# Kernel tuning notes

Hardware: AMD Instinct MI355X
Metric: run time of the kernel (lower is better)

## Reference

```python
import jax, jax.numpy as jnp
import numpy as np

B, N, D, H = 2, 4096, 256, 8
HD = D // H
NEG_SLOPE = 0.01
LN_EPS = 1e-5


def setup_inputs() -> dict:
    key = jax.random.key(0)
    ks = jax.random.split(key, 6)
    s = 1.0 / np.sqrt(D)
    return {
        "h": jax.random.normal(ks[0], (B, N, D), dtype=jnp.float32),
        "W_l": jax.random.normal(ks[1], (D, D), dtype=jnp.float32) * s,
        "W_r": jax.random.normal(ks[2], (D, D), dtype=jnp.float32) * s,
        "a_l": jax.random.normal(ks[3], (HD,), dtype=jnp.float32) * s,
        "a_r": jax.random.normal(ks[4], (HD,), dtype=jnp.float32) * s,
        "W_final": jax.random.normal(ks[5], (D, D), dtype=jnp.float32) * s,
        "ln_g": jnp.ones((D,), dtype=jnp.float32),
        "ln_b": jnp.zeros((D,), dtype=jnp.float32),
    }


def _leaky(x):
    return jnp.where(x >= 0, x, NEG_SLOPE * x)


def reference(h, W_l, W_r, a_l, a_r, W_final, ln_g, ln_b):
    b, n, d = h.shape
    # projections -> [b, H, n, HD]
    fl = (h @ W_l).reshape(b, n, H, HD).transpose(0, 2, 1, 3)
    fr = (h @ W_r).reshape(b, n, H, HD).transpose(0, 2, 1, 3)
    # additive GAT-style scores: [b, H, n] each, broadcast to [b, H, n, n]
    sl = jnp.einsum("bhnd,d->bhn", _leaky(fl), a_l)
    sr = jnp.einsum("bhnd,d->bhn", _leaky(fr), a_r)
    score = sl[..., :, None] + sr[..., None, :]  # [b, H, n, n]
    attn = jnp.mean(score, axis=1)  # pre-softmax mean over heads: [b, n, n]
    p = jax.nn.softmax(score, axis=-1)  # dropout is identity (eval / p=0)
    context = jnp.einsum("bhij,bhjd->bhid", p, fr)  # [b, H, n, HD]
    h_sa = context.transpose(0, 2, 1, 3).reshape(b, n, d)
    fh = h_sa @ W_final
    x = h + fh
    mu = jnp.mean(x, axis=-1, keepdims=True)
    var = jnp.mean(jnp.square(x - mu), axis=-1, keepdims=True)
    h_out = (x - mu) * jax.lax.rsqrt(var + LN_EPS) * ln_g + ln_b
    return (h_out, attn)
```

## Files before the change

kernel.cpp:

```cpp
#include <hip/hip_runtime.h>
#include <hip/hip_bf16.h>

#define BATCH 2
#define SEQ   4096
#define DIM   256
#define HEADS 8
#define HDIM  32
#define M_ROWS (BATCH * SEQ)
#define JCHUNK 32
#define NCHUNK (SEQ / JCHUNK)
#define CTXBLKS (BATCH * NCHUNK)
#define FPSCALE 4294967296.0

typedef short bf16x8 __attribute__((ext_vector_type(8)));
typedef unsigned short u16x8 __attribute__((ext_vector_type(8)));
typedef float f32x4 __attribute__((ext_vector_type(4)));

static __device__ inline unsigned short f2bf(float x) {
  union { float f; unsigned u; } v; v.f = x;
  unsigned r = v.u + 0x7FFF + ((v.u >> 16) & 1);
  return (unsigned short)(r >> 16);
}

__global__ __launch_bounds__(256) void k_prep(const float* __restrict__ Wl,
                                              const float* __restrict__ Wr,
                                              unsigned short* __restrict__ Wt,
                                              unsigned long long* __restrict__ yacc,
                                              unsigned long long* __restrict__ wacc) {
  if (blockIdx.y == 0) {
    const int idx = blockIdx.x * 256 + threadIdx.x;
    yacc[2 * idx] = 0ull;
    yacc[2 * idx + 1] = 0ull;
    if (idx < BATCH * HEADS) wacc[idx] = 0ull;
  }
  __shared__ float tile[32][33];
  const int k0 = blockIdx.x * 32;
  const int n0 = blockIdx.y * 32;
  const int t = threadIdx.x;
  const float* W = (n0 < 256) ? Wl : Wr;
  const int nb = n0 & 255;
  {
    const int r = t >> 3;
    const int c = (t & 7) * 4;
    const float4 v = *(const float4*)(&W[(size_t)(k0 + r) * DIM + nb + c]);
    tile[r][c + 0] = v.x; tile[r][c + 1] = v.y;
    tile[r][c + 2] = v.z; tile[r][c + 3] = v.w;
  }
  __syncthreads();
  {
    const int nl = t >> 3;
    const int kl = (t & 7) * 4;
    ushort4 o;
    o.x = f2bf(tile[kl + 0][nl]); o.y = f2bf(tile[kl + 1][nl]);
    o.z = f2bf(tile[kl + 2][nl]); o.w = f2bf(tile[kl + 3][nl]);
    *(ushort4*)(&Wt[(size_t)(n0 + nl) * DIM + k0 + kl]) = o;
  }
}

__global__ __launch_bounds__(512) void k_gemm_fused(
    const float* __restrict__ A, const unsigned short* __restrict__ Wt,
    const float* __restrict__ a_l, const float* __restrict__ a_r,
    float* __restrict__ fr, float* __restrict__ sr,
    float* __restrict__ msl, float* __restrict__ msr) {
  __shared__ unsigned short As[64 * 32];
  __shared__ unsigned short Bs[256 * 32];
  __shared__ float red[64][8];

  const int bid = blockIdx.x;
  const int isR = bid & 1;
  const int bm  = bid >> 1;
  const int m0 = bm * 64;
  const int n0 = isR * 256;

  const int t = threadIdx.x;
  const int lane = t & 63;
  const int wid = t >> 6;

  f32x4 acc[4][2];
  #pragma unroll
  for (int i = 0; i < 4; ++i)
    #pragma unroll
    for (int j = 0; j < 2; ++j) acc[i][j] = (f32x4){0.f, 0.f, 0.f, 0.f};

  for (int k0 = 0; k0 < DIM; k0 += 32) {
    if (t < 256) {
      const int row = t >> 2;
      const int kc = t & 3;
      const int slot = kc ^ ((row >> 1) & 3);
      const float4 a0 = *(const float4*)(&A[(size_t)(m0 + row) * DIM + k0 + kc * 8]);
      const float4 a1 = *(const float4*)(&A[(size_t)(m0 + row) * DIM + k0 + kc * 8 + 4]);
      u16x8 pa;
      pa[0] = f2bf(a0.x); pa[1] = f2bf(a0.y); pa[2] = f2bf(a0.z); pa[3] = f2bf(a0.w);
      pa[4] = f2bf(a1.x); pa[5] = f2bf(a1.y); pa[6] = f2bf(a1.z); pa[7] = f2bf(a1.w);
      *(u16x8*)((char*)As + row * 64 + slot * 16) = pa;
    }
    #pragma unroll
    for (int p = 0; p < 2; ++p) {
      const int task = t + p * 512;
      const int row = task >> 2;
      const int kc = task & 3;
      const int slot = kc ^ ((row >> 1) & 3);
      const u16x8 pb = *(const u16x8*)(&Wt[(size_t)(n0 + row) * DIM + k0 + kc * 8]);
      *(u16x8*)((char*)Bs + row * 64 + slot * 16) = pb;
    }
    __syncthreads();

    bf16x8 af[4], bfr[2];
    #pragma unroll
    for (int mr = 0; mr < 4; ++mr) {
      const int ra = mr * 16 + (lane & 15);
      const int sl = (lane >> 4) ^ ((ra >> 1) & 3);
      af[mr] = *(const bf16x8*)((const char*)As + ra * 64 + sl * 16);
    }
    #pragma unroll
    for (int nr = 0; nr < 2; ++nr) {
      const int cb = wid * 32 + nr * 16 + (lane & 15);
      const int sl = (lane >> 4) ^ ((cb >> 1) & 3);
      bfr[nr] = *(const bf16x8*)((const char*)Bs + cb * 64 + sl * 16);
    }
    #pragma unroll
    for (int mr = 0; mr < 4; ++mr)
      #pragma unroll
      for (int nr = 0; nr < 2; ++nr)
        acc[mr][nr] = __builtin_amdgcn_mfma_f32_16x16x32_bf16(af[mr], bfr[nr], acc[mr][nr], 0, 0, 0);
    __syncthreads();
  }

  const float* av = isR ? a_r : a_l;
  const int b = m0 >> 12;
  const int nbase = m0 & 4095;

  #pragma unroll
  for (int mr = 0; mr < 4; ++mr) {
    #pragma unroll
    for (int r = 0; r < 4; ++r) {
      float p = 0.f;
      #pragma unroll
      for (int nr = 0; nr < 2; ++nr) {
        float x = acc[mr][nr][r];
        x = x >= 0.f ? x : 0.01f * x;
        p = fmaf(x, av[nr * 16 + (lane & 15)], p);
      }
      #pragma unroll
      for (int o = 1; o < 16; o <<= 1) p += __shfl_xor(p, o, 16);
      if ((lane & 15) == 0) {
        const int rl = mr * 16 + (lane >> 4) * 4 + r;
        red[rl][wid] = p;
        if (isR) sr[((size_t)(b * HEADS + wid)) * SEQ + nbase + rl] = p;
      }
    }
  }
  __syncthreads();
  if (t < 64) {
    float s = 0.f;
    #pragma unroll
    for (int h2 = 0; h2 < 8; ++h2) s += red[t][h2];
    (isR ? msr : msl)[m0 + t] = s * 0.125f;
  }
  if (isR) {
    #pragma unroll
    for (int mr = 0; mr < 4; ++mr)
      #pragma unroll
      for (int nr = 0; nr < 2; ++nr) {
        const int col = wid * 32 + nr * 16 + (lane & 15);
        #pragma unroll
        for (int r = 0; r < 4; ++r) {
          const int row = m0 + mr * 16 + (lane >> 4) * 4 + r;
          fr[(size_t)row * DIM + col] = acc[mr][nr][r];
        }
      }
  }
}

__global__ __launch_bounds__(256) void k_mega(const float* __restrict__ sr,
                                              const float* __restrict__ fr,
                                              const float* __restrict__ Wf,
                                              const float* __restrict__ msl,
                                              const float* __restrict__ msr,
                                              unsigned long long* __restrict__ yacc,
                                              unsigned long long* __restrict__ wacc,
                                              float* __restrict__ attn) {
  const int blk = blockIdx.x;
  const int t = threadIdx.x;

  if (blk < CTXBLKS) {
    __shared__ float ws_[HEADS][JCHUNK];
    __shared__ float cps[DIM];
    const int b  = blk >> 7;
    const int jc = blk & 127;
    const int j0 = jc * JCHUNK;
    {
      const int h2 = t >> 5, jj = t & 31;
      float e = expf(sr[((size_t)(b * HEADS + h2)) * SEQ + j0 + jj]);
      ws_[h2][jj] = e;
      float s = e;
      #pragma unroll
      for (int o = 16; o > 0; o >>= 1) s += __shfl_xor(s, o, 32);
      if (jj == 0)
        atomicAdd(&wacc[b * HEADS + h2],
                  (unsigned long long)__double2ll_rn((double)s * FPSCALE));
    }
    __syncthreads();
    {
      const int h2 = t >> 5;
      const float* frb = fr + (size_t)(b * SEQ + j0) * DIM + t;
      float accv = 0.f;
      #pragma unroll 8
      for (int jj = 0; jj < JCHUNK; ++jj)
        accv = fmaf(ws_[h2][jj], frb[(size_t)jj * DIM], accv);
      cps[t] = accv;
    }
    __syncthreads();
    #pragma unroll
    for (int h2 = 0; h2 < HEADS; ++h2) {
      float yh = 0.f;
      #pragma unroll 8
      for (int d = 0; d < HDIM; ++d)
        yh = fmaf(cps[h2 * HDIM + d], Wf[(size_t)(h2 * HDIM + d) * DIM + t], yh);
      atomicAdd(&yacc[(size_t)(b * HEADS + h2) * DIM + t],
                (unsigned long long)__double2ll_rn((double)yh * FPSCALE));
    }
  } else {
    const int pr = blk - CTXBLKS;
    const int row0 = pr * 2;
    const int b = row0 >> 12;
    const float v0 = msl[row0];
    const float v1 = msl[row0 + 1];
    const f32x4* mr4 = (const f32x4*)(msr + ((size_t)b << 12));
    f32x4* dst0 = (f32x4*)(attn + ((size_t)row0 << 12));
    f32x4* dst1 = (f32x4*)(attn + ((size_t)(row0 + 1) << 12));
    #pragma unroll
    for (int q = 0; q < 4; ++q) {
      const f32x4 m4 = mr4[q * 256 + t];
      __builtin_nontemporal_store(m4 + v0, &dst0[q * 256 + t]);
      __builtin_nontemporal_store(m4 + v1, &dst1[q * 256 + t]);
    }
  }
}

__global__ __launch_bounds__(256) void k_ln(const float* __restrict__ h,
                                            const unsigned long long* __restrict__ yacc,
                                            const unsigned long long* __restrict__ wacc,
                                            const float* __restrict__ g,
                                            const float* __restrict__ bb,
                                            float* __restrict__ out) {
  const int pr = blockIdx.x;
  const int row0 = pr * 2;
  const int b = row0 >> 12;
  const int t = threadIdx.x;

  float fh = 0.f;
  #pragma unroll
  for (int h2 = 0; h2 < HEADS; ++h2) {
    const double yv = (double)(long long)yacc[(size_t)(b * HEADS + h2) * DIM + t];
    const double wv = (double)(long long)wacc[b * HEADS + h2];
    fh += (float)(yv / wv);
  }

  const float x0 = h[(size_t)row0 * DIM + t] + fh;
  const float x1 = h[(size_t)(row0 + 1) * DIM + t] + fh;
  float s10 = x0, s20 = x0 * x0, s11 = x1, s21 = x1 * x1;
  #pragma unroll
  for (int o = 32; o > 0; o >>= 1) {
    s10 += __shfl_xor(s10, o, 64);
    s20 += __shfl_xor(s20, o, 64);
    s11 += __shfl_xor(s11, o, 64);
    s21 += __shfl_xor(s21, o, 64);
  }
  __shared__ float r1[2][4], r2[2][4];
  if ((t & 63) == 0) {
    r1[0][t >> 6] = s10; r2[0][t >> 6] = s20;
    r1[1][t >> 6] = s11; r2[1][t >> 6] = s21;
  }
  __syncthreads();
  const float gs = g[t], bs = bb[t];
  {
    const float s1 = r1[0][0] + r1[0][1] + r1[0][2] + r1[0][3];
    const float s2 = r2[0][0] + r2[0][1] + r2[0][2] + r2[0][3];
    const float mu = s1 * (1.f / 256.f);
    const float var = s2 * (1.f / 256.f) - mu * mu;
    const float rs = rsqrtf(var + 1e-5f);
    out[(size_t)row0 * DIM + t] = (x0 - mu) * rs * gs + bs;
  }
  {
    const float s1 = r1[1][0] + r1[1][1] + r1[1][2] + r1[1][3];
    const float s2 = r2[1][0] + r2[1][1] + r2[1][2] + r2[1][3];
    const float mu = s1 * (1.f / 256.f);
    const float var = s2 * (1.f / 256.f) - mu * mu;
    const float rs = rsqrtf(var + 1e-5f);
    out[(size_t)(row0 + 1) * DIM + t] = (x1 - mu) * rs * gs + bs;
  }
}

extern "C" void kernel_launch(void* const* d_in, const int* in_sizes, int n_in,
                              void* d_out, int out_size, void* d_ws, size_t ws_size,
                              hipStream_t stream) {
  const float* h  = (const float*)d_in[0];
  const float* Wl = (const float*)d_in[1];
  const float* Wr = (const float*)d_in[2];
  const float* al = (const float*)d_in[3];
  const float* ar = (const float*)d_in[4];
  const float* Wf = (const float*)d_in[5];
  const float* g  = (const float*)d_in[6];
  const float* bb = (const float*)d_in[7];
  float* out = (float*)d_out;

  unsigned long long* yacc = (unsigned long long*)d_ws;
  unsigned long long* wacc = yacc + BATCH * HEADS * DIM;
  float* fr  = (float*)(wacc + BATCH * HEADS);
  float* srs = fr + (size_t)M_ROWS * DIM;
  float* msl = srs + BATCH * HEADS * SEQ;
  float* msr = msl + M_ROWS;
  unsigned short* Wt = (unsigned short*)(msr + M_ROWS);

  k_prep<<<dim3(8, 16), 256, 0, stream>>>(Wl, Wr, Wt, yacc, wacc);
  k_gemm_fused<<<256, 512, 0, stream>>>(h, Wt, al, ar, fr, srs, msl, msr);
  k_mega<<<CTXBLKS + M_ROWS / 2, 256, 0, stream>>>(srs, fr, Wf, msl, msr,
                                                   yacc, wacc,
                                                   out + (size_t)M_ROWS * DIM);
  k_ln<<<M_ROWS / 2, 256, 0, stream>>>(h, yacc, wacc, g, bb, out);
}
```

Baseline: 68.53 us.

## Double-buffer GEMM smem, move attn write into LN kernel, enlarge context chunk

Adds register-prefetched double buffering of the A/B tiles in the projection GEMM, so global loads for the next k-step overlap MFMA work and one barrier per step is removed. The context reduction moves to its own kernel with 64-row chunks, which halves the block count and the atomic traffic. The large attn broadcast write moves into the LayerNorm kernel, which now runs one row per block. This trades a parallel mega-kernel for fewer atomics and a combined output pass, but the attn write no longer overlaps the context computation.

Result: faster. 61.87 us (-9.7%).

```diff
diff --git a/kernel.cpp b/kernel.cpp
--- a/kernel.cpp
+++ b/kernel.cpp
@@ -7,7 +7,7 @@
 #define HEADS 8
 #define HDIM  32
 #define M_ROWS (BATCH * SEQ)
-#define JCHUNK 32
+#define JCHUNK 64
 #define NCHUNK (SEQ / JCHUNK)
 #define CTXBLKS (BATCH * NCHUNK)
 #define FPSCALE 4294967296.0
@@ -62,8 +62,8 @@
     const float* __restrict__ a_l, const float* __restrict__ a_r,
     float* __restrict__ fr, float* __restrict__ sr,
     float* __restrict__ msl, float* __restrict__ msr) {
-  __shared__ unsigned short As[64 * 32];
-  __shared__ unsigned short Bs[256 * 32];
+  __shared__ unsigned short As2[2][64 * 32];
+  __shared__ unsigned short Bs2[2][256 * 32];
   __shared__ float red[64][8];
 
   const int bid = blockIdx.x;
@@ -76,53 +76,79 @@
   const int lane = t & 63;
   const int wid = t >> 6;
 
+  const int arow = t >> 2;
+  const int akc  = t & 3;
+  const int aslot = akc ^ ((arow >> 1) & 3);
+  const int brow = t >> 2;
+  const int bkc  = t & 3;
+  const int bslot = bkc ^ ((brow >> 1) & 3);
+
+  float4 a0r, a1r;
+  u16x8 b0r, b1r;
+
+  if (t < 256) {
+    a0r = *(const float4*)(&A[(size_t)(m0 + arow) * DIM + akc * 8]);
+    a1r = *(const float4*)(&A[(size_t)(m0 + arow) * DIM + akc * 8 + 4]);
+  }
+  b0r = *(const u16x8*)(&Wt[(size_t)(n0 + brow) * DIM + bkc * 8]);
+  b1r = *(const u16x8*)(&Wt[(size_t)(n0 + 128 + brow) * DIM + bkc * 8]);
+  if (t < 256) {
+    u16x8 pa;
+    pa[0] = f2bf(a0r.x); pa[1] = f2bf(a0r.y); pa[2] = f2bf(a0r.z); pa[3] = f2bf(a0r.w);
+    pa[4] = f2bf(a1r.x); pa[5] = f2bf(a1r.y); pa[6] = f2bf(a1r.z); pa[7] = f2bf(a1r.w);
+    *(u16x8*)((char*)As2[0] + arow * 64 + aslot * 16) = pa;
+  }
+  *(u16x8*)((char*)Bs2[0] + brow * 64 + bslot * 16) = b0r;
+  *(u16x8*)((char*)Bs2[0] + (128 + brow) * 64 + bslot * 16) = b1r;
+  __syncthreads();
+
   f32x4 acc[4][2];
   #pragma unroll
   for (int i = 0; i < 4; ++i)
     #pragma unroll
     for (int j = 0; j < 2; ++j) acc[i][j] = (f32x4){0.f, 0.f, 0.f, 0.f};
 
-  for (int k0 = 0; k0 < DIM; k0 += 32) {
-    if (t < 256) {
-      const int row = t >> 2;
-      const int kc = t & 3;
-      const int slot = kc ^ ((row >> 1) & 3);
-      const float4 a0 = *(const float4*)(&A[(size_t)(m0 + row) * DIM + k0 + kc * 8]);
-      const float4 a1 = *(const float4*)(&A[(size_t)(m0 + row) * DIM + k0 + kc * 8 + 4]);
-      u16x8 pa;
-      pa[0] = f2bf(a0.x); pa[1] = f2bf(a0.y); pa[2] = f2bf(a0.z); pa[3] = f2bf(a0.w);
-      pa[4] = f2bf(a1.x); pa[5] = f2bf(a1.y); pa[6] = f2bf(a1.z); pa[7] = f2bf(a1.w);
-      *(u16x8*)((char*)As + row * 64 + slot * 16) = pa;
-    }
-    #pragma unroll
-    for (int p = 0; p < 2; ++p) {
-      const int task = t + p * 512;
-      const int row = task >> 2;
-      const int kc = task & 3;
-      const int slot = kc ^ ((row >> 1) & 3);
-      const u16x8 pb = *(const u16x8*)(&Wt[(size_t)(n0 + row) * DIM + k0 + kc * 8]);
-      *(u16x8*)((char*)Bs + row * 64 + slot * 16) = pb;
-    }
-    __syncthreads();
+  for (int ks = 0; ks < 8; ++ks) {
+    const int cur = ks & 1;
+    if (ks < 7) {
+      const int k0 = (ks + 1) * 32;
+      if (t < 256) {
+        a0r = *(const float4*)(&A[(size_t)(m0 + arow) * DIM + k0 + akc * 8]);
+        a1r = *(const float4*)(&A[(size_t)(m0 + arow) * DIM + k0 + akc * 8 + 4]);
+      }
+      b0r = *(const u16x8*)(&Wt[(size_t)(n0 + brow) * DIM + k0 + bkc * 8]);
+      b1r = *(const u16x8*)(&Wt[(size_t)(n0 + 128 + brow) * DIM + k0 + bkc * 8]);
+    }
 
     bf16x8 af[4], bfr[2];
     #pragma unroll
     for (int mr = 0; mr < 4; ++mr) {
       const int ra = mr * 16 + (lane & 15);
       const int sl = (lane >> 4) ^ ((ra >> 1) & 3);
-      af[mr] = *(const bf16x8*)((const char*)As + ra * 64 + sl * 16);
+      af[mr] = *(const bf16x8*)((const char*)As2[cur] + ra * 64 + sl * 16);
     }
     #pragma unroll
     for (int nr = 0; nr < 2; ++nr) {
       const int cb = wid * 32 + nr * 16 + (lane & 15);
       const int sl = (lane >> 4) ^ ((cb >> 1) & 3);
-      bfr[nr] = *(const bf16x8*)((const char*)Bs + cb * 64 + sl * 16);
+      bfr[nr] = *(const bf16x8*)((const char*)Bs2[cur] + cb * 64 + sl * 16);
     }
     #pragma unroll
     for (int mr = 0; mr < 4; ++mr)
       #pragma unroll
       for (int nr = 0; nr < 2; ++nr)
         acc[mr][nr] = __builtin_amdgcn_mfma_f32_16x16x32_bf16(af[mr], bfr[nr], acc[mr][nr], 0, 0, 0);
+
+    if (ks < 7) {
+      if (t < 256) {
+        u16x8 pa;
+        pa[0] = f2bf(a0r.x); pa[1] = f2bf(a0r.y); pa[2] = f2bf(a0r.z); pa[3] = f2bf(a0r.w);
+        pa[4] = f2bf(a1r.x); pa[5] = f2bf(a1r.y); pa[6] = f2bf(a1r.z); pa[7] = f2bf(a1r.w);
+        *(u16x8*)((char*)As2[cur ^ 1] + arow * 64 + aslot * 16) = pa;
+      }
+      *(u16x8*)((char*)Bs2[cur ^ 1] + brow * 64 + bslot * 16) = b0r;
+      *(u16x8*)((char*)Bs2[cur ^ 1] + (128 + brow) * 64 + bslot * 16) = b1r;
+    }
     __syncthreads();
   }
 
@@ -172,123 +198,102 @@
   }
 }
 
-__global__ __launch_bounds__(256) void k_mega(const float* __restrict__ sr,
-                                              const float* __restrict__ fr,
-                                              const float* __restrict__ Wf,
-                                              const float* __restrict__ msl,
-                                              const float* __restrict__ msr,
-                                              unsigned long long* __restrict__ yacc,
-                                              unsigned long long* __restrict__ wacc,
-                                              float* __restrict__ attn) {
+__global__ __launch_bounds__(256) void k_ctx(const float* __restrict__ sr,
+                                             const float* __restrict__ fr,
+                                             const float* __restrict__ Wf,
+                                             unsigned long long* __restrict__ yacc,
+                                             unsigned long long* __restrict__ wacc) {
   const int blk = blockIdx.x;
+  const int b  = blk >> 6;
+  const int jc = blk & 63;
+  const int j0 = jc * JCHUNK;
   const int t = threadIdx.x;
-
-  if (blk < CTXBLKS) {
-    __shared__ float ws_[HEADS][JCHUNK];
-    __shared__ float cps[DIM];
-    const int b  = blk >> 7;
-    const int jc = blk & 127;
-    const int j0 = jc * JCHUNK;
-    {
-      const int h2 = t >> 5, jj = t & 31;
-      float e = expf(sr[((size_t)(b * HEADS + h2)) * SEQ + j0 + jj]);
-      ws_[h2][jj] = e;
-      float s = e;
-      #pragma unroll
-      for (int o = 16; o > 0; o >>= 1) s += __shfl_xor(s, o, 32);
-      if (jj == 0)
-        atomicAdd(&wacc[b * HEADS + h2],
-                  (unsigned long long)__double2ll_rn((double)s * FPSCALE));
-    }
-    __syncthreads();
-    {
-      const int h2 = t >> 5;
-      const float* frb = fr + (size_t)(b * SEQ + j0) * DIM + t;
-      float accv = 0.f;
-      #pragma unroll 8
-      for (int jj = 0; jj < JCHUNK; ++jj)
-        accv = fmaf(ws_[h2][jj], frb[(size_t)jj * DIM], accv);
-      cps[t] = accv;
-    }
-    __syncthreads();
-    #pragma unroll
-    for (int h2 = 0; h2 < HEADS; ++h2) {
-      float yh = 0.f;
-      #pragma unroll 8
-      for (int d = 0; d < HDIM; ++d)
-        yh = fmaf(cps[h2 * HDIM + d], Wf[(size_t)(h2 * HDIM + d) * DIM + t], yh);
-      atomicAdd(&yacc[(size_t)(b * HEADS + h2) * DIM + t],
-                (unsigned long long)__double2ll_rn((double)yh * FPSCALE));
-    }
-  } else {
-    const int pr = blk - CTXBLKS;
-    const int row0 = pr * 2;
-    const int b = row0 >> 12;
-    const float v0 = msl[row0];
-    const float v1 = msl[row0 + 1];
-    const f32x4* mr4 = (const f32x4*)(msr + ((size_t)b << 12));
-    f32x4* dst0 = (f32x4*)(attn + ((size_t)row0 << 12));
-    f32x4* dst1 = (f32x4*)(attn + ((size_t)(row0 + 1) << 12));
-    #pragma unroll
-    for (int q = 0; q < 4; ++q) {
-      const f32x4 m4 = mr4[q * 256 + t];
-      __builtin_nontemporal_store(m4 + v0, &dst0[q * 256 + t]);
-      __builtin_nontemporal_store(m4 + v1, &dst1[q * 256 + t]);
-    }
-  }
-}
-
-__global__ __launch_bounds__(256) void k_ln(const float* __restrict__ h,
-                                            const unsigned long long* __restrict__ yacc,
-                                            const unsigned long long* __restrict__ wacc,
-                                            const float* __restrict__ g,
-                                            const float* __restrict__ bb,
-                                            float* __restrict__ out) {
-  const int pr = blockIdx.x;
-  const int row0 = pr * 2;
-  const int b = row0 >> 12;
+  __shared__ float ws_[HEADS][JCHUNK];
+  __shared__ float cps[DIM];
+
+  {
+    const int h2 = t >> 5, jj = t & 31;
+    const float* sb = sr + ((size_t)(b * HEADS + h2)) * SEQ + j0;
+    const float e0 = expf(sb[jj]);
+    const float e1 = expf(sb[jj + 32]);
+    ws_[h2][jj] = e0;
+    ws_[h2][jj + 32] = e1;
+    float s = e0 + e1;
+    #pragma unroll
+    for (int o = 16; o > 0; o >>= 1) s += __shfl_xor(s, o, 32);
+    if (jj == 0)
+      atomicAdd(&wacc[b * HEADS + h2],
+                (unsigned long long)__double2ll_rn((double)s * FPSCALE));
+  }
+  __syncthreads();
+  {
+    const int h2 = t >> 5;
+    const float* frb = fr + (size_t)(b * SEQ + j0) * DIM + t;
+    float accv = 0.f;
+    #pragma unroll 8
+    for (int jj = 0; jj < JCHUNK; ++jj)
+      accv = fmaf(ws_[h2][jj], frb[(size_t)jj * DIM], accv);
+    cps[t] = accv;
+  }
+  __syncthreads();
+  #pragma unroll
+  for (int h3 = 0; h3 < HEADS; ++h3) {
+    float yh = 0.f;
+    #pragma unroll 8
+    for (int d = 0; d < HDIM; ++d)
+      yh = fmaf(cps[h3 * HDIM + d], Wf[(size_t)(h3 * HDIM + d) * DIM + t], yh);
+    atomicAdd(&yacc[(size_t)(b * HEADS + h3) * DIM + t],
+              (unsigned long long)__double2ll_rn((double)yh * FPSCALE));
+  }
+}
+
+__global__ __launch_bounds__(256) void k_ln_attn(const float* __restrict__ h,
+                                                 const unsigned long long* __restrict__ yacc,
+                                                 const unsigned long long* __restrict__ wacc,
+                                                 const float* __restrict__ g,
+                                                 const float* __restrict__ bb,
+                                                 const float* __restrict__ msl,
+                                                 const float* __restrict__ msr,
+                                                 float* __restrict__ out,
+                                                 float* __restrict__ attn) {
+  const int row = blockIdx.x;
+  const int b = row >> 12;
   const int t = threadIdx.x;
+  __shared__ float winv[HEADS];
+  if (t < HEADS)
+    winv[t] = (float)(1.0 / (double)(long long)wacc[b * HEADS + t]);
+  __syncthreads();
 
   float fh = 0.f;
   #pragma unroll
-  for (int h2 = 0; h2 < HEADS; ++h2) {
-    const double yv = (double)(long long)yacc[(size_t)(b * HEADS + h2) * DIM + t];
-    const double wv = (double)(long long)wacc[b * HEADS + h2];
-    fh += (float)(yv / wv);
-  }
-
-  const float x0 = h[(size_t)row0 * DIM + t] + fh;
-  const float x1 = h[(size_t)(row0 + 1) * DIM + t] + fh;
-  float s10 = x0, s20 = x0 * x0, s11 = x1, s21 = x1 * x1;
+  for (int h2 = 0; h2 < HEADS; ++h2)
+    fh = fmaf((float)(long long)yacc[(size_t)(b * HEADS + h2) * DIM + t],
+              winv[h2], fh);
+
+  const float x = h[(size_t)row * DIM + t] + fh;
+  float s1 = x, s2 = x * x;
   #pragma unroll
   for (int o = 32; o > 0; o >>= 1) {
-    s10 += __shfl_xor(s10, o, 64);
-    s20 += __shfl_xor(s20, o, 64);
-    s11 += __shfl_xor(s11, o, 64);
-    s21 += __shfl_xor(s21, o, 64);
-  }
-  __shared__ float r1[2][4], r2[2][4];
-  if ((t & 63) == 0) {
-    r1[0][t >> 6] = s10; r2[0][t >> 6] = s20;
-    r1[1][t >> 6] = s11; r2[1][t >> 6] = s21;
-  }
-  __syncthreads();
-  const float gs = g[t], bs = bb[t];
-  {
-    const float s1 = r1[0][0] + r1[0][1] + r1[0][2] + r1[0][3];
-    const float s2 = r2[0][0] + r2[0][1] + r2[0][2] + r2[0][3];
-    const float mu = s1 * (1.f / 256.f);
-    const float var = s2 * (1.f / 256.f) - mu * mu;
-    const float rs = rsqrtf(var + 1e-5f);
-    out[(size_t)row0 * DIM + t] = (x0 - mu) * rs * gs + bs;
-  }
-  {
-    const float s1 = r1[1][0] + r1[1][1] + r1[1][2] + r1[1][3];
-    const float s2 = r2[1][0] + r2[1][1] + r2[1][2] + r2[1][3];
-    const float mu = s1 * (1.f / 256.f);
-    const float var = s2 * (1.f / 256.f) - mu * mu;
-    const float rs = rsqrtf(var + 1e-5f);
-    out[(size_t)(row0 + 1) * DIM + t] = (x1 - mu) * rs * gs + bs;
+    s1 += __shfl_xor(s1, o, 64);
+    s2 += __shfl_xor(s2, o, 64);
+  }
+  __shared__ float r1[4], r2[4];
+  if ((t & 63) == 0) { r1[t >> 6] = s1; r2[t >> 6] = s2; }
+  __syncthreads();
+  s1 = r1[0] + r1[1] + r1[2] + r1[3];
+  s2 = r2[0] + r2[1] + r2[2] + r2[3];
+  const float mu = s1 * (1.f / 256.f);
+  const float var = s2 * (1.f / 256.f) - mu * mu;
+  const float rs = rsqrtf(var + 1e-5f);
+  out[(size_t)row * DIM + t] = (x - mu) * rs * g[t] + bb[t];
+
+  const float v = msl[row];
+  const f32x4* mr4 = (const f32x4*)(msr + ((size_t)b << 12));
+  f32x4* dst = (f32x4*)(attn + ((size_t)row << 12));
+  #pragma unroll
+  for (int q = 0; q < 4; ++q) {
+    const f32x4 m4 = mr4[q * 256 + t];
+    __builtin_nontemporal_store(m4 + v, &dst[q * 256 + t]);
   }
 }
 
@@ -315,8 +320,7 @@
 
   k_prep<<<dim3(8, 16), 256, 0, stream>>>(Wl, Wr, Wt, yacc, wacc);
   k_gemm_fused<<<256, 512, 0, stream>>>(h, Wt, al, ar, fr, srs, msl, msr);
-  k_mega<<<CTXBLKS + M_ROWS / 2, 256, 0, stream>>>(srs, fr, Wf, msl, msr,
-                                                   yacc, wacc,
-                                                   out + (size_t)M_ROWS * DIM);
-  k_ln<<<M_ROWS / 2, 256, 0, stream>>>(h, yacc, wacc, g, bb, out);
-}
+  k_ctx<<<CTXBLKS, 256, 0, stream>>>(srs, fr, Wf, yacc, wacc);
+  k_ln_attn<<<M_ROWS, 256, 0, stream>>>(h, yacc, wacc, g, bb, msl, msr,
+                                        out, out + (size_t)M_ROWS * DIM);
+}
```
